# Performance work log

Hardware: AMD Instinct MI355X
Metric: run time of the kernel (lower is better)

Reference implementation:

```python
import jax, jax.numpy as jnp
import numpy as np


def setup_inputs() -> dict:
    key = jax.random.key(0)
    k1, k2 = jax.random.split(key)
    x = jax.random.normal(k1, (32, 256, 32, 32), dtype=jnp.float32)
    emb = jax.random.uniform(k2, (256, 2048), dtype=jnp.float32)
    return {"x": x, "emb": emb}


def reference(x, emb):
    # x: (B, D, H, W), emb: (D, K)
    B, D = x.shape[0], x.shape[1]
    spatial = x.shape[2:]
    K = emb.shape[1]
    # flatten latents: (N, D) with N = B*H*W
    xf = jnp.moveaxis(x, 1, -1).reshape(-1, D)
    d2 = (jnp.sum(xf * xf, axis=-1, keepdims=True)
          - 2.0 * (xf @ emb)
          + jnp.sum(emb * emb, axis=0))  # (N, K)
    argmin = jnp.argmin(d2, axis=-1)  # (N,)
    q = jnp.take(emb.T, argmin, axis=0)  # (N, D) nearest codes
    out = q.reshape(B, *spatial, D)
    out = jnp.moveaxis(out, -1, 1)  # (B, D, H, W)
    return out
```

## Files before the change

### kernel.cpp

```cpp
#include <hip/hip_runtime.h>


typedef __attribute__((ext_vector_type(8))) _Float16 half8v;
typedef __attribute__((ext_vector_type(16))) float floatx16;
typedef unsigned int uint;
typedef unsigned short ushort;

#define DD 256
#define KK 2048
#define SS 1024
#define NN 32768
#define MT 128
#define NTT 256
#define LDA 24
#define MFMA_F16 __builtin_amdgcn_mfma_f32_32x32x16_f16

#define EPLANE 262144

union HU { _Float16 f; ushort u; };

__device__ __forceinline__ void split16(float v, ushort& h, ushort& l) {
    HU a, b;
    a.f = (_Float16)v;
    b.f = (_Float16)(v - (float)a.f);
    h = a.u; l = b.u;
}

__global__ __launch_bounds__(256) void hn_kernel(const float* __restrict__ emb,
                                                 float* __restrict__ hn) {
    __shared__ float red[256];
    const int tid = threadIdx.x;
    const int k = blockIdx.x * 32 + (tid & 31);
    const int j = tid >> 5;
    float a = 0.f;
#pragma unroll
    for (int i = 0; i < 32; ++i) {
        float e = emb[(size_t)(j * 32 + i) * KK + k];
        a += e * e;
    }
    red[tid] = a;
    __syncthreads();
    if (j == 0) {
        float s = a;
#pragma unroll
        for (int g = 1; g < 8; ++g) s += red[g * 32 + (tid & 31)];
        hn[k] = 0.5f * s;
    }
}

__global__ __launch_bounds__(256) void pack_emb(const float* __restrict__ emb,
                                                uint* __restrict__ epk) {
    int idx = blockIdx.x * 256 + threadIdx.x;
    int k = idx & (KK - 1);
    int d2 = idx >> 11;
    float a = emb[(size_t)(2 * d2) * KK + k];
    float b = emb[(size_t)(2 * d2 + 1) * KK + k];
    ushort h0, l0, h1, l1;
    split16(a, h0, l0);
    split16(b, h1, l1);
    epk[idx] = (uint)h0 | ((uint)h1 << 16);
    epk[EPLANE + idx] = (uint)l0 | ((uint)l1 << 16);
}

template <bool PRE>
__global__ __launch_bounds__(1024, 4) void vq_fused(
        const float* __restrict__ x, const float* __restrict__ emb,
        const float* __restrict__ hn, const uint* __restrict__ epk,
        float* __restrict__ out) {
    __shared__ ushort Ah[2][MT * LDA], Al[2][MT * LDA];
    __shared__ ushort Bh[2][NTT * LDA], Bl[2][NTT * LDA];
    __shared__ float sv[4][MT];
    __shared__ int   sc[4][MT];
    __shared__ int   bc[MT];

    const int tid = threadIdx.x;
    const int lane = tid & 63;
    const int wid = tid >> 6;
    const int colk = lane & 31;
    const int half = lane >> 5;
    const int wm = (wid & 3) * 32;
    const int wn = (wid >> 2) * 64;

    const int base_n = blockIdx.x * MT;
    const int bq = base_n >> 10;
    const int sb = base_n & (SS - 1);

    const int lat_a = tid & 127;
    const int d2a = tid >> 7;
    const int cod_b = tid & 255;
    const int qb = tid >> 8;

    const float* xA = x + ((size_t)bq * DD + 2 * d2a) * SS + sb + lat_a;

    floatx16 acc[2];
#pragma unroll
    for (int j = 0; j < 2; ++j) acc[j] = (floatx16)(0.0f);

    float bestv[16];
    int bestc[16];
#pragma unroll
    for (int r = 0; r < 16; ++r) { bestv[r] = 3.4e38f; bestc[r] = 0; }

    float fa[2];
    uint ub[4];
    float fb[4];

    fa[0] = xA[0];
    fa[1] = xA[SS];
    if constexpr (PRE) {
        const uint* uB = epk + (size_t)(2 * qb) * KK + cod_b;
        ub[0] = uB[0];
        ub[1] = uB[KK];
        ub[2] = uB[EPLANE];
        ub[3] = uB[EPLANE + KK];
    } else {
        const float* p = emb + (size_t)(4 * qb) * KK + cod_b;
#pragma unroll
        for (int i = 0; i < 4; ++i) fb[i] = p[(size_t)i * KK];
    }
    {
        ushort h0, l0, h1, l1;
        split16(fa[0], h0, l0);
        split16(fa[1], h1, l1);
        *reinterpret_cast<uint*>(&Ah[0][lat_a * LDA + 2 * d2a]) =
            (uint)h0 | ((uint)h1 << 16);
        *reinterpret_cast<uint*>(&Al[0][lat_a * LDA + 2 * d2a]) =
            (uint)l0 | ((uint)l1 << 16);
        uint2 wh, wl;
        if constexpr (PRE) {
            wh.x = ub[0]; wh.y = ub[1];
            wl.x = ub[2]; wl.y = ub[3];
        } else {
            ushort h[4], l[4];
#pragma unroll
            for (int i = 0; i < 4; ++i) split16(fb[i], h[i], l[i]);
            wh.x = (uint)h[0] | ((uint)h[1] << 16);
            wh.y = (uint)h[2] | ((uint)h[3] << 16);
            wl.x = (uint)l[0] | ((uint)l[1] << 16);
            wl.y = (uint)l[2] | ((uint)l[3] << 16);
        }
        *reinterpret_cast<uint2*>(&Bh[0][cod_b * LDA + 4 * qb]) = wh;
        *reinterpret_cast<uint2*>(&Bl[0][cod_b * LDA + 4 * qb]) = wl;
    }
    __syncthreads();

    for (int c = 0; c < 128; ++c) {
        const int cur = c & 1, nxt = cur ^ 1;
        if (c < 127) {
            const int c1 = c + 1;
            const int kt1 = c1 >> 4;
            const int dt1 = (c1 & 15) * 16;
            fa[0] = xA[(size_t)dt1 * SS];
            fa[1] = xA[(size_t)dt1 * SS + SS];
            if constexpr (PRE) {
                const uint* uB = epk + (size_t)(dt1 / 2 + 2 * qb) * KK
                                 + kt1 * NTT + cod_b;
                ub[0] = uB[0];
                ub[1] = uB[KK];
                ub[2] = uB[EPLANE];
                ub[3] = uB[EPLANE + KK];
            } else {
                const float* p = emb + (size_t)(dt1 + 4 * qb) * KK
                                 + kt1 * NTT + cod_b;
#pragma unroll
                for (int i = 0; i < 4; ++i) fb[i] = p[(size_t)i * KK];
            }
        }
        const int fo = colk * LDA + half * 8;
        half8v ah = *reinterpret_cast<const half8v*>(&Ah[cur][fo + wm * LDA]);
        half8v al = *reinterpret_cast<const half8v*>(&Al[cur][fo + wm * LDA]);
        half8v bh0 = *reinterpret_cast<const half8v*>(&Bh[cur][fo + wn * LDA]);
        half8v bh1 = *reinterpret_cast<const half8v*>(&Bh[cur][fo + (wn + 32) * LDA]);
        half8v bl0 = *reinterpret_cast<const half8v*>(&Bl[cur][fo + wn * LDA]);
        half8v bl1 = *reinterpret_cast<const half8v*>(&Bl[cur][fo + (wn + 32) * LDA]);

        acc[0] = MFMA_F16(ah, bh0, acc[0], 0, 0, 0);
        acc[0] = MFMA_F16(ah, bl0, acc[0], 0, 0, 0);
        acc[0] = MFMA_F16(al, bh0, acc[0], 0, 0, 0);

        acc[1] = MFMA_F16(ah, bh1, acc[1], 0, 0, 0);
        acc[1] = MFMA_F16(ah, bl1, acc[1], 0, 0, 0);
        acc[1] = MFMA_F16(al, bh1, acc[1], 0, 0, 0);

        if (c < 127) {
            ushort h0, l0, h1, l1;
            split16(fa[0], h0, l0);
            split16(fa[1], h1, l1);
            *reinterpret_cast<uint*>(&Ah[nxt][lat_a * LDA + 2 * d2a]) =
                (uint)h0 | ((uint)h1 << 16);
            *reinterpret_cast<uint*>(&Al[nxt][lat_a * LDA + 2 * d2a]) =
                (uint)l0 | ((uint)l1 << 16);
            uint2 wh, wl;
            if constexpr (PRE) {
                wh.x = ub[0]; wh.y = ub[1];
                wl.x = ub[2]; wl.y = ub[3];
            } else {
                ushort h[4], l[4];
#pragma unroll
                for (int i = 0; i < 4; ++i) split16(fb[i], h[i], l[i]);
                wh.x = (uint)h[0] | ((uint)h[1] << 16);
                wh.y = (uint)h[2] | ((uint)h[3] << 16);
                wl.x = (uint)l[0] | ((uint)l[1] << 16);
                wl.y = (uint)l[2] | ((uint)l[3] << 16);
            }
            *reinterpret_cast<uint2*>(&Bh[nxt][cod_b * LDA + 4 * qb]) = wh;
            *reinterpret_cast<uint2*>(&Bl[nxt][cod_b * LDA + 4 * qb]) = wl;
        }
        if ((c & 15) == 15) {
            const int kt = c >> 4;
            const int cd0 = kt * NTT + wn + colk;
            const int cd1 = cd0 + 32;
            const float h0 = hn[cd0];
            const float h1 = hn[cd1];
#pragma unroll
            for (int r = 0; r < 16; ++r) {
                float s0 = h0 - acc[0][r];
                float s1 = h1 - acc[1][r];
                float v = s0; int cd = cd0;
                if (s1 < s0) { v = s1; cd = cd1; }
                if (v < bestv[r]) { bestv[r] = v; bestc[r] = cd; }
                acc[0][r] = 0.f;
                acc[1][r] = 0.f;
            }
        }
        __syncthreads();
    }

#pragma unroll
    for (int r = 0; r < 16; ++r) {
        float v = bestv[r];
        int cd = bestc[r];
#pragma unroll
        for (int mk = 1; mk < 32; mk <<= 1) {
            float ov = __shfl_xor(v, mk);
            int oc = __shfl_xor(cd, mk);
            if (ov < v || (ov == v && oc < cd)) { v = ov; cd = oc; }
        }
        if (colk == 0) {
            const int row = (r & 3) + 8 * (r >> 2) + 4 * half;
            sv[wid >> 2][wm + row] = v;
            sc[wid >> 2][wm + row] = cd;
        }
    }
    __syncthreads();
    if (tid < MT) {
        float v = sv[0][tid]; int cd = sc[0][tid];
#pragma unroll
        for (int g = 1; g < 4; ++g) {
            float ov = sv[g][tid]; int oc = sc[g][tid];
            if (ov < v || (ov == v && oc < cd)) { v = ov; cd = oc; }
        }
        bc[tid] = cd;
    }
    __syncthreads();
    {
        const int mq = tid & 31;
        const int dg = tid >> 5;
        const int k0 = bc[mq * 4 + 0];
        const int k1 = bc[mq * 4 + 1];
        const int k2 = bc[mq * 4 + 2];
        const int k3 = bc[mq * 4 + 3];
#pragma unroll 4
        for (int dd = 0; dd < 8; ++dd) {
            const int d = dg * 8 + dd;
            const float* er = emb + (size_t)d * KK;
            float4 o = make_float4(er[k0], er[k1], er[k2], er[k3]);
            reinterpret_cast<float4*>(&out[((size_t)bq * DD + d) * SS + sb])[mq] = o;
        }
    }
}

extern "C" void kernel_launch(void* const* d_in, const int* in_sizes, int n_in,
                              void* d_out, int out_size, void* d_ws, size_t ws_size,
                              hipStream_t stream) {
    const float* x = (const float*)d_in[0];
    const float* emb = (const float*)d_in[1];
    float* out = (float*)d_out;
    float* hn = (float*)d_ws;
    uint* epk = (uint*)((char*)d_ws + KK * sizeof(float));

    const size_t need = (size_t)KK * 4 + (size_t)2 * EPLANE * 4;

    hipLaunchKernelGGL(hn_kernel, dim3(KK / 32), dim3(256), 0, stream, emb, hn);
    if (ws_size >= need) {
        hipLaunchKernelGGL(pack_emb, dim3(EPLANE / 256), dim3(256), 0, stream,
                           emb, epk);
        hipLaunchKernelGGL((vq_fused<true>), dim3(NN / MT), dim3(1024), 0, stream,
                           x, emb, hn, epk, out);
    } else {
        hipLaunchKernelGGL((vq_fused<false>), dim3(NN / MT), dim3(1024), 0, stream,
                           x, emb, hn, epk, out);
    }
}
```

Before: 235.9 us.

## Double K-chunk depth per stage and pack embedding in 8-wide uint4 planes

Each pipeline stage now covers 32 channels instead of 16, which halves the number of main-loop iterations and barriers per codebook tile. The precomputed fp16 hi/lo embedding is repacked into uint4 groups of 8 channels, so each thread loads two 16-byte words and writes a full row segment to LDS with vector stores. The LDS row stride grows to 40 halves to fit the wider chunk. In exchange, LDS use and register pressure per thread go up, which could lower occupancy.

```diff
diff --git a/kernel.cpp b/kernel.cpp
--- a/kernel.cpp
+++ b/kernel.cpp
@@ -12,10 +12,9 @@
 #define NN 32768
 #define MT 128
 #define NTT 256
-#define LDA 24
+#define CD 32
+#define LDA 40
 #define MFMA_F16 __builtin_amdgcn_mfma_f32_32x32x16_f16
-
-#define EPLANE 262144
 
 union HU { _Float16 f; ushort u; };
 
@@ -24,6 +23,10 @@
     a.f = (_Float16)v;
     b.f = (_Float16)(v - (float)a.f);
     h = a.u; l = b.u;
+}
+
+__device__ __forceinline__ uint pk(ushort a, ushort b) {
+    return (uint)a | ((uint)b << 16);
 }
 
 __global__ __launch_bounds__(256) void hn_kernel(const float* __restrict__ emb,
@@ -49,23 +52,29 @@
 }
 
 __global__ __launch_bounds__(256) void pack_emb(const float* __restrict__ emb,
-                                                uint* __restrict__ epk) {
+                                                uint4* __restrict__ epk) {
     int idx = blockIdx.x * 256 + threadIdx.x;
     int k = idx & (KK - 1);
-    int d2 = idx >> 11;
-    float a = emb[(size_t)(2 * d2) * KK + k];
-    float b = emb[(size_t)(2 * d2 + 1) * KK + k];
-    ushort h0, l0, h1, l1;
-    split16(a, h0, l0);
-    split16(b, h1, l1);
-    epk[idx] = (uint)h0 | ((uint)h1 << 16);
-    epk[EPLANE + idx] = (uint)l0 | ((uint)l1 << 16);
+    int q = idx >> 11;
+    ushort h[8], l[8];
+#pragma unroll
+    for (int j = 0; j < 8; ++j) {
+        float e = emb[(size_t)(8 * q + j) * KK + k];
+        split16(e, h[j], l[j]);
+    }
+    uint4 H, L;
+    H.x = pk(h[0], h[1]); H.y = pk(h[2], h[3]);
+    H.z = pk(h[4], h[5]); H.w = pk(h[6], h[7]);
+    L.x = pk(l[0], l[1]); L.y = pk(l[2], l[3]);
+    L.z = pk(l[4], l[5]); L.w = pk(l[6], l[7]);
+    epk[(size_t)(q * 2 + 0) * KK + k] = H;
+    epk[(size_t)(q * 2 + 1) * KK + k] = L;
 }
 
 template <bool PRE>
 __global__ __launch_bounds__(1024, 4) void vq_fused(
         const float* __restrict__ x, const float* __restrict__ emb,
-        const float* __restrict__ hn, const uint* __restrict__ epk,
+        const float* __restrict__ hn, const uint4* __restrict__ epk,
         float* __restrict__ out) {
     __shared__ ushort Ah[2][MT * LDA], Al[2][MT * LDA];
     __shared__ ushort Bh[2][NTT * LDA], Bl[2][NTT * LDA];
@@ -88,7 +97,8 @@
     const int lat_a = tid & 127;
     const int d2a = tid >> 7;
     const int cod_b = tid & 255;
-    const int qb = tid >> 8;
+    const int pB = (tid >> 8) & 1;
+    const int oB = tid >> 9;
 
     const float* xA = x + ((size_t)bq * DD + 2 * d2a) * SS + sb + lat_a;
 
@@ -101,113 +111,129 @@
 #pragma unroll
     for (int r = 0; r < 16; ++r) { bestv[r] = 3.4e38f; bestc[r] = 0; }
 
-    float fa[2];
-    uint ub[4];
-    float fb[4];
+    float fa[4];
+    uint4 ub0, ub1;
+    float fb[16];
 
     fa[0] = xA[0];
     fa[1] = xA[SS];
+    fa[2] = xA[(size_t)16 * SS];
+    fa[3] = xA[(size_t)17 * SS];
     if constexpr (PRE) {
-        const uint* uB = epk + (size_t)(2 * qb) * KK + cod_b;
-        ub[0] = uB[0];
-        ub[1] = uB[KK];
-        ub[2] = uB[EPLANE];
-        ub[3] = uB[EPLANE + KK];
+        const int qg = 2 * oB;
+        ub0 = epk[(size_t)(qg * 2 + pB) * KK + cod_b];
+        ub1 = epk[(size_t)((qg + 1) * 2 + pB) * KK + cod_b];
     } else {
-        const float* p = emb + (size_t)(4 * qb) * KK + cod_b;
-#pragma unroll
-        for (int i = 0; i < 4; ++i) fb[i] = p[(size_t)i * KK];
+#pragma unroll
+        for (int i = 0; i < 16; ++i)
+            fb[i] = emb[(size_t)(oB * 16 + i) * KK + cod_b];
     }
     {
-        ushort h0, l0, h1, l1;
-        split16(fa[0], h0, l0);
-        split16(fa[1], h1, l1);
-        *reinterpret_cast<uint*>(&Ah[0][lat_a * LDA + 2 * d2a]) =
-            (uint)h0 | ((uint)h1 << 16);
-        *reinterpret_cast<uint*>(&Al[0][lat_a * LDA + 2 * d2a]) =
-            (uint)l0 | ((uint)l1 << 16);
-        uint2 wh, wl;
+        ushort h0, l0, h1, l1, h2, l2, h3, l3;
+        split16(fa[0], h0, l0); split16(fa[1], h1, l1);
+        split16(fa[2], h2, l2); split16(fa[3], h3, l3);
+        *reinterpret_cast<uint*>(&Ah[0][lat_a * LDA + 2 * d2a]) = pk(h0, h1);
+        *reinterpret_cast<uint*>(&Al[0][lat_a * LDA + 2 * d2a]) = pk(l0, l1);
+        *reinterpret_cast<uint*>(&Ah[0][lat_a * LDA + 2 * d2a + 16]) = pk(h2, h3);
+        *reinterpret_cast<uint*>(&Al[0][lat_a * LDA + 2 * d2a + 16]) = pk(l2, l3);
+        uint4 w0, w1;
         if constexpr (PRE) {
-            wh.x = ub[0]; wh.y = ub[1];
-            wl.x = ub[2]; wl.y = ub[3];
+            w0 = ub0; w1 = ub1;
         } else {
-            ushort h[4], l[4];
-#pragma unroll
-            for (int i = 0; i < 4; ++i) split16(fb[i], h[i], l[i]);
-            wh.x = (uint)h[0] | ((uint)h[1] << 16);
-            wh.y = (uint)h[2] | ((uint)h[3] << 16);
-            wl.x = (uint)l[0] | ((uint)l[1] << 16);
-            wl.y = (uint)l[2] | ((uint)l[3] << 16);
-        }
-        *reinterpret_cast<uint2*>(&Bh[0][cod_b * LDA + 4 * qb]) = wh;
-        *reinterpret_cast<uint2*>(&Bl[0][cod_b * LDA + 4 * qb]) = wl;
+            ushort h[16], l[16];
+#pragma unroll
+            for (int i = 0; i < 16; ++i) split16(fb[i], h[i], l[i]);
+            const ushort* s = pB ? l : h;
+            w0.x = pk(s[0], s[1]);  w0.y = pk(s[2], s[3]);
+            w0.z = pk(s[4], s[5]);  w0.w = pk(s[6], s[7]);
+            w1.x = pk(s[8], s[9]);  w1.y = pk(s[10], s[11]);
+            w1.z = pk(s[12], s[13]); w1.w = pk(s[14], s[15]);
+        }
+        ushort* Bp = pB ? &Bl[0][0] : &Bh[0][0];
+        *reinterpret_cast<uint4*>(&Bp[cod_b * LDA + oB * 16]) = w0;
+        *reinterpret_cast<uint4*>(&Bp[cod_b * LDA + oB * 16 + 8]) = w1;
     }
     __syncthreads();
 
-    for (int c = 0; c < 128; ++c) {
+    for (int c = 0; c < 64; ++c) {
         const int cur = c & 1, nxt = cur ^ 1;
-        if (c < 127) {
+        if (c < 63) {
             const int c1 = c + 1;
-            const int kt1 = c1 >> 4;
-            const int dt1 = (c1 & 15) * 16;
-            fa[0] = xA[(size_t)dt1 * SS];
-            fa[1] = xA[(size_t)dt1 * SS + SS];
+            const int kt1 = c1 >> 3;
+            const int dt1 = (c1 & 7) * CD;
+            fa[0] = xA[(size_t)(dt1 + 0) * SS];
+            fa[1] = xA[(size_t)(dt1 + 1) * SS];
+            fa[2] = xA[(size_t)(dt1 + 16) * SS];
+            fa[3] = xA[(size_t)(dt1 + 17) * SS];
             if constexpr (PRE) {
-                const uint* uB = epk + (size_t)(dt1 / 2 + 2 * qb) * KK
-                                 + kt1 * NTT + cod_b;
-                ub[0] = uB[0];
-                ub[1] = uB[KK];
-                ub[2] = uB[EPLANE];
-                ub[3] = uB[EPLANE + KK];
+                const int qg = (dt1 >> 3) + 2 * oB;
+                const size_t kb = (size_t)kt1 * NTT + cod_b;
+                ub0 = epk[(size_t)(qg * 2 + pB) * KK + kb];
+                ub1 = epk[(size_t)((qg + 1) * 2 + pB) * KK + kb];
             } else {
-                const float* p = emb + (size_t)(dt1 + 4 * qb) * KK
-                                 + kt1 * NTT + cod_b;
-#pragma unroll
-                for (int i = 0; i < 4; ++i) fb[i] = p[(size_t)i * KK];
+#pragma unroll
+                for (int i = 0; i < 16; ++i)
+                    fb[i] = emb[(size_t)(dt1 + oB * 16 + i) * KK
+                                + kt1 * NTT + cod_b];
             }
         }
         const int fo = colk * LDA + half * 8;
-        half8v ah = *reinterpret_cast<const half8v*>(&Ah[cur][fo + wm * LDA]);
-        half8v al = *reinterpret_cast<const half8v*>(&Al[cur][fo + wm * LDA]);
-        half8v bh0 = *reinterpret_cast<const half8v*>(&Bh[cur][fo + wn * LDA]);
-        half8v bh1 = *reinterpret_cast<const half8v*>(&Bh[cur][fo + (wn + 32) * LDA]);
-        half8v bl0 = *reinterpret_cast<const half8v*>(&Bl[cur][fo + wn * LDA]);
-        half8v bl1 = *reinterpret_cast<const half8v*>(&Bl[cur][fo + (wn + 32) * LDA]);
-
-        acc[0] = MFMA_F16(ah, bh0, acc[0], 0, 0, 0);
-        acc[0] = MFMA_F16(ah, bl0, acc[0], 0, 0, 0);
-        acc[0] = MFMA_F16(al, bh0, acc[0], 0, 0, 0);
-
-        acc[1] = MFMA_F16(ah, bh1, acc[1], 0, 0, 0);
-        acc[1] = MFMA_F16(ah, bl1, acc[1], 0, 0, 0);
-        acc[1] = MFMA_F16(al, bh1, acc[1], 0, 0, 0);
-
-        if (c < 127) {
-            ushort h0, l0, h1, l1;
-            split16(fa[0], h0, l0);
-            split16(fa[1], h1, l1);
-            *reinterpret_cast<uint*>(&Ah[nxt][lat_a * LDA + 2 * d2a]) =
-                (uint)h0 | ((uint)h1 << 16);
-            *reinterpret_cast<uint*>(&Al[nxt][lat_a * LDA + 2 * d2a]) =
-                (uint)l0 | ((uint)l1 << 16);
-            uint2 wh, wl;
+        {
+            half8v ah = *reinterpret_cast<const half8v*>(&Ah[cur][fo + wm * LDA]);
+            half8v al = *reinterpret_cast<const half8v*>(&Al[cur][fo + wm * LDA]);
+            half8v bh0 = *reinterpret_cast<const half8v*>(&Bh[cur][fo + wn * LDA]);
+            half8v bh1 = *reinterpret_cast<const half8v*>(&Bh[cur][fo + (wn + 32) * LDA]);
+            half8v bl0 = *reinterpret_cast<const half8v*>(&Bl[cur][fo + wn * LDA]);
+            half8v bl1 = *reinterpret_cast<const half8v*>(&Bl[cur][fo + (wn + 32) * LDA]);
+            acc[0] = MFMA_F16(ah, bh0, acc[0], 0, 0, 0);
+            acc[0] = MFMA_F16(ah, bl0, acc[0], 0, 0, 0);
+            acc[0] = MFMA_F16(al, bh0, acc[0], 0, 0, 0);
+            acc[1] = MFMA_F16(ah, bh1, acc[1], 0, 0, 0);
+            acc[1] = MFMA_F16(ah, bl1, acc[1], 0, 0, 0);
+            acc[1] = MFMA_F16(al, bh1, acc[1], 0, 0, 0);
+        }
+        {
+            half8v ah = *reinterpret_cast<const half8v*>(&Ah[cur][fo + wm * LDA + 16]);
+            half8v al = *reinterpret_cast<const half8v*>(&Al[cur][fo + wm * LDA + 16]);
+            half8v bh0 = *reinterpret_cast<const half8v*>(&Bh[cur][fo + wn * LDA + 16]);
+            half8v bh1 = *reinterpret_cast<const half8v*>(&Bh[cur][fo + (wn + 32) * LDA + 16]);
+            half8v bl0 = *reinterpret_cast<const half8v*>(&Bl[cur][fo + wn * LDA + 16]);
+            half8v bl1 = *reinterpret_cast<const half8v*>(&Bl[cur][fo + (wn + 32) * LDA + 16]);
+            acc[0] = MFMA_F16(ah, bh0, acc[0], 0, 0, 0);
+            acc[0] = MFMA_F16(ah, bl0, acc[0], 0, 0, 0);
+            acc[0] = MFMA_F16(al, bh0, acc[0], 0, 0, 0);
+            acc[1] = MFMA_F16(ah, bh1, acc[1], 0, 0, 0);
+            acc[1] = MFMA_F16(ah, bl1, acc[1], 0, 0, 0);
+            acc[1] = MFMA_F16(al, bh1, acc[1], 0, 0, 0);
+        }
+
+        if (c < 63) {
+            ushort h0, l0, h1, l1, h2, l2, h3, l3;
+            split16(fa[0], h0, l0); split16(fa[1], h1, l1);
+            split16(fa[2], h2, l2); split16(fa[3], h3, l3);
+            *reinterpret_cast<uint*>(&Ah[nxt][lat_a * LDA + 2 * d2a]) = pk(h0, h1);
+            *reinterpret_cast<uint*>(&Al[nxt][lat_a * LDA + 2 * d2a]) = pk(l0, l1);
+            *reinterpret_cast<uint*>(&Ah[nxt][lat_a * LDA + 2 * d2a + 16]) = pk(h2, h3);
+            *reinterpret_cast<uint*>(&Al[nxt][lat_a * LDA + 2 * d2a + 16]) = pk(l2, l3);
+            uint4 w0, w1;
             if constexpr (PRE) {
-                wh.x = ub[0]; wh.y = ub[1];
-                wl.x = ub[2]; wl.y = ub[3];
+                w0 = ub0; w1 = ub1;
             } else {
-                ushort h[4], l[4];
-#pragma unroll
-                for (int i = 0; i < 4; ++i) split16(fb[i], h[i], l[i]);
-                wh.x = (uint)h[0] | ((uint)h[1] << 16);
-                wh.y = (uint)h[2] | ((uint)h[3] << 16);
-                wl.x = (uint)l[0] | ((uint)l[1] << 16);
-                wl.y = (uint)l[2] | ((uint)l[3] << 16);
+                ushort h[16], l[16];
+#pragma unroll
+                for (int i = 0; i < 16; ++i) split16(fb[i], h[i], l[i]);
+                const ushort* s = pB ? l : h;
+                w0.x = pk(s[0], s[1]);  w0.y = pk(s[2], s[3]);
+                w0.z = pk(s[4], s[5]);  w0.w = pk(s[6], s[7]);
+                w1.x = pk(s[8], s[9]);  w1.y = pk(s[10], s[11]);
+                w1.z = pk(s[12], s[13]); w1.w = pk(s[14], s[15]);
             }
-            *reinterpret_cast<uint2*>(&Bh[nxt][cod_b * LDA + 4 * qb]) = wh;
-            *reinterpret_cast<uint2*>(&Bl[nxt][cod_b * LDA + 4 * qb]) = wl;
-        }
-        if ((c & 15) == 15) {
-            const int kt = c >> 4;
+            ushort* Bp = pB ? &Bl[nxt][0] : &Bh[nxt][0];
+            *reinterpret_cast<uint4*>(&Bp[cod_b * LDA + oB * 16]) = w0;
+            *reinterpret_cast<uint4*>(&Bp[cod_b * LDA + oB * 16 + 8]) = w1;
+        }
+        if ((c & 7) == 7) {
+            const int kt = c >> 3;
             const int cd0 = kt * NTT + wn + colk;
             const int cd1 = cd0 + 32;
             const float h0 = hn[cd0];
@@ -277,13 +303,13 @@
     const float* emb = (const float*)d_in[1];
     float* out = (float*)d_out;
     float* hn = (float*)d_ws;
-    uint* epk = (uint*)((char*)d_ws + KK * sizeof(float));
-
-    const size_t need = (size_t)KK * 4 + (size_t)2 * EPLANE * 4;
+    uint4* epk = (uint4*)((char*)d_ws + KK * sizeof(float));
+
+    const size_t need = (size_t)KK * 4 + (size_t)32 * 2 * KK * 16;
 
     hipLaunchKernelGGL(hn_kernel, dim3(KK / 32), dim3(256), 0, stream, emb, hn);
     if (ws_size >= need) {
-        hipLaunchKernelGGL(pack_emb, dim3(EPLANE / 256), dim3(256), 0, stream,
+        hipLaunchKernelGGL(pack_emb, dim3(65536 / 256), dim3(256), 0, stream,
                            emb, epk);
         hipLaunchKernelGGL((vq_fused<true>), dim3(NN / MT), dim3(1024), 0, stream,
                            x, emb, hn, epk, out);
```

New measurement: 216.1 us. -8.4%, faster.
